# Performance work log

Hardware: AMD Instinct MI355X
Metric: run time of the kernel (lower is better)

Reference implementation:

```python
import jax, jax.numpy as jnp
import numpy as np

MARGIN = 0.3


def _l2norm(x, axis=-1):
    return x / (jnp.linalg.norm(x, axis=axis, keepdims=True) + 1e-12)


def setup_inputs() -> dict:
    key = jax.random.key(0)
    k1, k2, k3, k4 = jax.random.split(key, 4)
    n, P, d = 1024, 8, 2048
    global_feat = jax.random.normal(k1, (n, d), dtype=jnp.float32)
    partial_feat = jax.random.normal(k2, (n, P, d), dtype=jnp.float32)
    part_labels = jax.random.randint(k3, (n, P), 0, 2).astype(jnp.float32)
    global_labels = jax.random.randint(k4, (n,), 0, 64).astype(jnp.int64)
    return {"global_feat": global_feat, "partial_feat": partial_feat,
            "part_labels": part_labels, "global_labels": global_labels}


def reference(global_feat, partial_feat, part_labels, global_labels):
    # --- compute_distance (VGTripletLoss) ---
    g = _l2norm(global_feat)            # [n, d]
    p = _l2norm(partial_feat)           # [n, P, d]
    gs = (1.0 - g @ g.T) / 2.0          # [n, n]
    overlap = part_labels[:, None, :] * part_labels[None, :, :]   # [n, n, P]
    # per-part cosine distance: [n, n, P]
    slf = (1.0 - jnp.einsum('ipd,jpd->ijp', p, p)) / 2.0
    slf = slf * overlap
    dist = (slf.sum(-1) + gs) / (overlap.sum(-1) + 1.0)            # [n, n]

    # --- compute_loss: hard positive/negative mining ---
    mask = global_labels[:, None] == global_labels[None, :]        # [n, n]
    neg_inf = jnp.float32(-1e30)
    pos_inf = jnp.float32(1e30)
    dist_ap = jnp.max(jnp.where(mask, dist, neg_inf), axis=1)      # hardest positive
    dist_an = jnp.min(jnp.where(mask, pos_inf, dist), axis=1)      # hardest negative
    # MarginRankingLoss(y=1, reduction='mean'): max(0, dist_ap - dist_an + margin)
    loss = jnp.mean(jax.nn.relu(dist_ap - dist_an + MARGIN))
    return loss
```

## Files before the change

kernel.cpp:

```cpp
#include <hip/hip_runtime.h>

#define N 1024
#define D 2048
#define P 8
#define F 9
#define KTOT (F * D)
#define SPLIT 16
#define KS (KTOT / SPLIT)
#define BM 128
#define BKT 32
#define NITER (KS / BKT)
#define NTILE 36
#define MARGIN 0.3f

typedef float f32x4 __attribute__((ext_vector_type(4)));
typedef short s16x8 __attribute__((ext_vector_type(8)));

#define GLOBAL_AS __attribute__((address_space(1)))
#define LDS_AS __attribute__((address_space(3)))

__device__ __forceinline__ const float* feat_row(const float* __restrict__ g,
                                                 const float* __restrict__ p,
                                                 int i, int f) {
    return (f == 0) ? (g + (size_t)i * D)
                    : (p + ((size_t)i * P + (f - 1)) * D);
}

__device__ __forceinline__ unsigned f2bf(float x) {
    unsigned u = __float_as_uint(x);
    return (u + 0x7fffu + ((u >> 16) & 1u)) >> 16;
}

__device__ __forceinline__ void tile_map(int lid, int& bi, int& bj) {
    int rem = lid, r = 0;
    while (rem >= 8 - r) { rem -= 8 - r; ++r; }
    bi = r;
    bj = r + rem;
}

__global__ __launch_bounds__(256)
void pack_kernel(const float* __restrict__ gfeat,
                 const float* __restrict__ pfeat,
                 const float* __restrict__ plab,
                 unsigned short* __restrict__ V,
                 float* __restrict__ draw,
                 float* __restrict__ out) {
    {
        const int zi = blockIdx.x * 256 + threadIdx.x;
        if (zi < NTILE * BM * BM / 4)
            ((float4*)draw)[zi] = (float4){0.f, 0.f, 0.f, 0.f};
        if (zi == 0) out[0] = 0.f;
    }
    const int wave = threadIdx.x >> 6, lane = threadIdx.x & 63;
    const int r = blockIdx.x * 4 + wave;
    const int i = r / F, f = r % F;
    const float4* s4 = (const float4*)feat_row(gfeat, pfeat, i, f);
    float4 v[8];
    float ss = 0.f;
    #pragma unroll
    for (int q = 0; q < 8; ++q) {
        v[q] = s4[lane + 64 * q];
        ss += v[q].x*v[q].x + v[q].y*v[q].y + v[q].z*v[q].z + v[q].w*v[q].w;
    }
    #pragma unroll
    for (int m = 32; m >= 1; m >>= 1) ss += __shfl_xor(ss, m, 64);
    const float ls = (f == 0) ? 1.0f : plab[i * P + (f - 1)];
    const float inv = ls / (sqrtf(ss) + 1e-12f);
    #pragma unroll
    for (int q = 0; q < 8; ++q) {
        uint2 o;
        o.x = f2bf(v[q].x * inv) | (f2bf(v[q].y * inv) << 16);
        o.y = f2bf(v[q].z * inv) | (f2bf(v[q].w * inv) << 16);
        *(uint2*)&V[(size_t)r * D + (lane + 64 * q) * 4] = o;
    }
}

__global__ __launch_bounds__(256)
void gemm_kernel(const unsigned short* __restrict__ V,
                 float* __restrict__ draw) {
    __shared__ short As[2][BM * BKT];
    __shared__ short Bs[2][BM * BKT];

    const int t = threadIdx.x;
    const int wave = t >> 6, lane = t & 63;
    int bi, bj;
    tile_map(blockIdx.x, bi, bj);
    const bool diag = (bi == bj);
    const int i0 = bi * BM;
    const int j0 = bj * BM;
    const int kbase = blockIdx.y * KS;

    const unsigned short* Ap = V + (size_t)(i0 + (t >> 2)) * KTOT + kbase + (t & 3) * 8;
    const unsigned short* Bp = V + (size_t)(j0 + (t >> 2)) * KTOT + kbase + (t & 3) * 8;

    const int kq = lane >> 4;
    const int rA = (wave & 1) * 64 + (lane & 15);
    const int rB = (wave >> 1) * 64 + (lane & 15);

    f32x4 acc[4][4];
    #pragma unroll
    for (int m = 0; m < 4; ++m)
        #pragma unroll
        for (int n = 0; n < 4; ++n)
            acc[m][n] = (f32x4){0.f, 0.f, 0.f, 0.f};

    auto stage = [&](int buf, int ks) {
        __builtin_amdgcn_global_load_lds(
            (const GLOBAL_AS void*)(Ap + ks * BKT),
            (LDS_AS void*)(As[buf] + t * 8), 16, 0, 0);
        __builtin_amdgcn_global_load_lds(
            (const GLOBAL_AS void*)(Ap + ks * BKT + (size_t)64 * KTOT),
            (LDS_AS void*)(As[buf] + 2048 + t * 8), 16, 0, 0);
        if (!diag) {
            __builtin_amdgcn_global_load_lds(
                (const GLOBAL_AS void*)(Bp + ks * BKT),
                (LDS_AS void*)(Bs[buf] + t * 8), 16, 0, 0);
            __builtin_amdgcn_global_load_lds(
                (const GLOBAL_AS void*)(Bp + ks * BKT + (size_t)64 * KTOT),
                (LDS_AS void*)(Bs[buf] + 2048 + t * 8), 16, 0, 0);
        }
    };

    auto compute = [&](int buf) {
        const short* Abase = As[buf] + rA * BKT + kq * 8;
        const short* Bbase = (diag ? As[buf] : Bs[buf]) + rB * BKT + kq * 8;
        s16x8 af[4], bfr[4];
        #pragma unroll
        for (int m = 0; m < 4; ++m) af[m] = *(const s16x8*)(Abase + m * 16 * BKT);
        #pragma unroll
        for (int n = 0; n < 4; ++n) bfr[n] = *(const s16x8*)(Bbase + n * 16 * BKT);
        #pragma unroll
        for (int m = 0; m < 4; ++m)
            #pragma unroll
            for (int n = 0; n < 4; ++n)
                acc[m][n] = __builtin_amdgcn_mfma_f32_16x16x32_bf16(
                    af[m], bfr[n], acc[m][n], 0, 0, 0);
    };

    stage(0, 0);
    for (int kk = 0; kk < NITER; kk += 2) {
        __syncthreads();
        if (kk + 1 < NITER) stage(1, kk + 1);
        compute(0);
        __syncthreads();
        if (kk + 2 < NITER) stage(0, kk + 2);
        compute(1);
    }

    float* outp = draw + (size_t)blockIdx.x * BM * BM;
    const int rbase = (wave & 1) * 64 + (lane >> 4) * 4;
    const int cbase = (wave >> 1) * 64 + (lane & 15);
    #pragma unroll
    for (int m = 0; m < 4; ++m)
        #pragma unroll
        for (int n = 0; n < 4; ++n)
            #pragma unroll
            for (int r = 0; r < 4; ++r)
                unsafeAtomicAdd(&outp[(size_t)(rbase + m * 16 + r) * BM + cbase + n * 16],
                                acc[m][n][r]);
}

__global__ __launch_bounds__(256)
void mine_kernel(const float* __restrict__ draw,
                 const float* __restrict__ plab,
                 const int* __restrict__ glab,
                 float* __restrict__ out) {
    const int i = blockIdx.x;
    const int t = threadIdx.x;
    const int li = glab[i];
    const int bi = i >> 7, ri = i & 127;
    float lab_i[P];
    #pragma unroll
    for (int c = 0; c < P; ++c) lab_i[c] = plab[i * P + c];

    float ap = -1e30f, an = 1e30f;
    for (int j = t; j < N; j += 256) {
        const int bj = j >> 7, rj = j & 127;
        size_t idx;
        if (bi <= bj)
            idx = (size_t)(bi * (17 - bi) / 2 + (bj - bi)) * (BM * BM) + ri * BM + rj;
        else
            idx = (size_t)(bj * (17 - bj) / 2 + (bi - bj)) * (BM * BM) + rj * BM + ri;
        float raw = draw[idx];
        float ov = 0.f;
        #pragma unroll
        for (int c = 0; c < P; ++c) ov += lab_i[c] * plab[j * P + c];
        float d = 0.5f - raw / (2.0f * (ov + 1.0f));
        if (glab[j] == li) ap = fmaxf(ap, d);
        else               an = fminf(an, d);
    }
    __shared__ float smax[256], smin[256];
    smax[t] = ap; smin[t] = an;
    __syncthreads();
    for (int s = 128; s > 0; s >>= 1) {
        if (t < s) {
            smax[t] = fmaxf(smax[t], smax[t + s]);
            smin[t] = fminf(smin[t], smin[t + s]);
        }
        __syncthreads();
    }
    if (t == 0) {
        float loss = fmaxf(0.f, smax[0] - smin[0] + MARGIN);
        unsafeAtomicAdd(out, loss * (1.0f / N));
    }
}

extern "C" void kernel_launch(void* const* d_in, const int* in_sizes, int n_in,
                              void* d_out, int out_size, void* d_ws, size_t ws_size,
                              hipStream_t stream) {
    const float* gfeat = (const float*)d_in[0];
    const float* pfeat = (const float*)d_in[1];
    const float* plab  = (const float*)d_in[2];
    const int*   glab  = (const int*)d_in[3];
    float* out = (float*)d_out;

    char* ws = (char*)d_ws;
    unsigned short* V = (unsigned short*)ws;
    float* draw = (float*)(ws + (size_t)37748736);

    pack_kernel<<<(N * F) / 4, 256, 0, stream>>>(gfeat, pfeat, plab, V, draw, out);
    gemm_kernel<<<dim3(NTILE, SPLIT), 256, 0, stream>>>(V, draw);
    mine_kernel<<<N, 256, 0, stream>>>(draw, plab, glab, out);
}
```

Measured before the change: 200.7 us.

## Widen GEMM K-tile to 64 with XOR-swizzled LDS and single buffer

Doubles the K step per iteration to 64 and stages each tile through a single LDS buffer instead of double buffering. It XOR-swizzles the 16-byte chunk placement in LDS to avoid bank conflicts on the MFMA fragment reads. The goal is fewer barriers and loop iterations per K slice and conflict-free LDS reads. The trade-off is losing the overlap of global loads with compute, since each iteration now loads and then waits before computing.

Result: faster. 187.4 us (-6.6%).

```diff
diff --git a/kernel.cpp b/kernel.cpp
--- a/kernel.cpp
+++ b/kernel.cpp
@@ -8,7 +8,7 @@
 #define SPLIT 16
 #define KS (KTOT / SPLIT)
 #define BM 128
-#define BKT 32
+#define BKT 64
 #define NITER (KS / BKT)
 #define NTILE 36
 #define MARGIN 0.3f
@@ -78,8 +78,8 @@
 __global__ __launch_bounds__(256)
 void gemm_kernel(const unsigned short* __restrict__ V,
                  float* __restrict__ draw) {
-    __shared__ short As[2][BM * BKT];
-    __shared__ short Bs[2][BM * BKT];
+    __shared__ short As[BM * BKT];
+    __shared__ short Bs[BM * BKT];
 
     const int t = threadIdx.x;
     const int wave = t >> 6, lane = t & 63;
@@ -90,12 +90,19 @@
     const int j0 = bj * BM;
     const int kbase = blockIdx.y * KS;
 
-    const unsigned short* Ap = V + (size_t)(i0 + (t >> 2)) * KTOT + kbase + (t & 3) * 8;
-    const unsigned short* Bp = V + (size_t)(j0 + (t >> 2)) * KTOT + kbase + (t & 3) * 8;
+    const int srow0 = t >> 3;
+    const int schunk = (t & 7) ^ (srow0 & 7);
+    const unsigned short* Ap = V + (size_t)(i0 + srow0) * KTOT + kbase + schunk * 8;
+    const unsigned short* Bp = V + (size_t)(j0 + srow0) * KTOT + kbase + schunk * 8;
 
     const int kq = lane >> 4;
     const int rA = (wave & 1) * 64 + (lane & 15);
     const int rB = (wave >> 1) * 64 + (lane & 15);
+    const short* Ab0 = As + rA * BKT + ((kq    ) ^ (rA & 7)) * 8;
+    const short* Ab1 = As + rA * BKT + ((4 + kq) ^ (rA & 7)) * 8;
+    const short* Bsrc = diag ? As : Bs;
+    const short* Bb0 = Bsrc + rB * BKT + ((kq    ) ^ (rB & 7)) * 8;
+    const short* Bb1 = Bsrc + rB * BKT + ((4 + kq) ^ (rB & 7)) * 8;
 
     f32x4 acc[4][4];
     #pragma unroll
@@ -104,47 +111,50 @@
         for (int n = 0; n < 4; ++n)
             acc[m][n] = (f32x4){0.f, 0.f, 0.f, 0.f};
 
-    auto stage = [&](int buf, int ks) {
-        __builtin_amdgcn_global_load_lds(
-            (const GLOBAL_AS void*)(Ap + ks * BKT),
-            (LDS_AS void*)(As[buf] + t * 8), 16, 0, 0);
-        __builtin_amdgcn_global_load_lds(
-            (const GLOBAL_AS void*)(Ap + ks * BKT + (size_t)64 * KTOT),
-            (LDS_AS void*)(As[buf] + 2048 + t * 8), 16, 0, 0);
+    for (int ks = 0; ks < NITER; ++ks) {
+        __syncthreads();
+        #pragma unroll
+        for (int p = 0; p < 4; ++p)
+            __builtin_amdgcn_global_load_lds(
+                (const GLOBAL_AS void*)(Ap + (size_t)(32 * p) * KTOT),
+                (LDS_AS void*)(As + p * 2048 + t * 8), 16, 0, 0);
         if (!diag) {
-            __builtin_amdgcn_global_load_lds(
-                (const GLOBAL_AS void*)(Bp + ks * BKT),
-                (LDS_AS void*)(Bs[buf] + t * 8), 16, 0, 0);
-            __builtin_amdgcn_global_load_lds(
-                (const GLOBAL_AS void*)(Bp + ks * BKT + (size_t)64 * KTOT),
-                (LDS_AS void*)(Bs[buf] + 2048 + t * 8), 16, 0, 0);
-        }
-    };
-
-    auto compute = [&](int buf) {
-        const short* Abase = As[buf] + rA * BKT + kq * 8;
-        const short* Bbase = (diag ? As[buf] : Bs[buf]) + rB * BKT + kq * 8;
-        s16x8 af[4], bfr[4];
-        #pragma unroll
-        for (int m = 0; m < 4; ++m) af[m] = *(const s16x8*)(Abase + m * 16 * BKT);
-        #pragma unroll
-        for (int n = 0; n < 4; ++n) bfr[n] = *(const s16x8*)(Bbase + n * 16 * BKT);
-        #pragma unroll
-        for (int m = 0; m < 4; ++m)
-            #pragma unroll
-            for (int n = 0; n < 4; ++n)
-                acc[m][n] = __builtin_amdgcn_mfma_f32_16x16x32_bf16(
-                    af[m], bfr[n], acc[m][n], 0, 0, 0);
-    };
-
-    stage(0, 0);
-    for (int kk = 0; kk < NITER; kk += 2) {
+            #pragma unroll
+            for (int p = 0; p < 4; ++p)
+                __builtin_amdgcn_global_load_lds(
+                    (const GLOBAL_AS void*)(Bp + (size_t)(32 * p) * KTOT),
+                    (LDS_AS void*)(Bs + p * 2048 + t * 8), 16, 0, 0);
+        }
+        Ap += BKT;
+        Bp += BKT;
         __syncthreads();
-        if (kk + 1 < NITER) stage(1, kk + 1);
-        compute(0);
-        __syncthreads();
-        if (kk + 2 < NITER) stage(0, kk + 2);
-        compute(1);
+
+        {
+            s16x8 af[4], bfr[4];
+            #pragma unroll
+            for (int m = 0; m < 4; ++m) af[m] = *(const s16x8*)(Ab0 + m * 16 * BKT);
+            #pragma unroll
+            for (int n = 0; n < 4; ++n) bfr[n] = *(const s16x8*)(Bb0 + n * 16 * BKT);
+            #pragma unroll
+            for (int m = 0; m < 4; ++m)
+                #pragma unroll
+                for (int n = 0; n < 4; ++n)
+                    acc[m][n] = __builtin_amdgcn_mfma_f32_16x16x32_bf16(
+                        af[m], bfr[n], acc[m][n], 0, 0, 0);
+        }
+        {
+            s16x8 af[4], bfr[4];
+            #pragma unroll
+            for (int m = 0; m < 4; ++m) af[m] = *(const s16x8*)(Ab1 + m * 16 * BKT);
+            #pragma unroll
+            for (int n = 0; n < 4; ++n) bfr[n] = *(const s16x8*)(Bb1 + n * 16 * BKT);
+            #pragma unroll
+            for (int m = 0; m < 4; ++m)
+                #pragma unroll
+                for (int n = 0; n < 4; ++n)
+                    acc[m][n] = __builtin_amdgcn_mfma_f32_16x16x32_bf16(
+                        af[m], bfr[n], acc[m][n], 0, 0, 0);
+        }
     }
 
     float* outp = draw + (size_t)blockIdx.x * BM * BM;
```
